# Kernel tuning notes

Measured on AMD Instinct MI355X. Metric: run time of the kernel, lower is better.

The kernel has to match this reference:

```python
import jax, jax.numpy as jnp
import numpy as np

D_MODEL = 2048
N_HEADS = 32
N_KV = 8
D_K = D_MODEL // N_HEADS  # 64
N_REP = N_HEADS // N_KV   # 4


def setup_inputs() -> dict:
    key = jax.random.key(0)
    ks = jax.random.split(key, 5)
    B, T = 2, 2048
    s = 0.02
    return {
        "x": jax.random.normal(ks[0], (B, T, D_MODEL), dtype=jnp.float32),
        "Wq": jax.random.normal(ks[1], (D_MODEL, D_MODEL), dtype=jnp.float32) * s,
        "Wk": jax.random.normal(ks[2], (N_KV * D_K, D_MODEL), dtype=jnp.float32) * s,
        "Wv": jax.random.normal(ks[3], (N_KV * D_K, D_MODEL), dtype=jnp.float32) * s,
        "Wo": jax.random.normal(ks[4], (D_MODEL, D_MODEL), dtype=jnp.float32) * s,
    }


def reference(x, Wq, Wk, Wv, Wo):
    B, T, C = x.shape
    # projections (torch Linear: x @ W.T)
    Q = (x @ Wq.T).reshape(B, T, N_KV, N_REP, D_K)  # group query heads by kv group
    K = (x @ Wk.T).reshape(B, T, N_KV, D_K)
    V = (x @ Wv.T).reshape(B, T, N_KV, D_K)
    scale = 1.0 / jnp.sqrt(jnp.asarray(D_K, dtype=x.dtype))
    # scores: (B, n_kv, n_rep, T, T) == repeated-KV scores without materializing repeats
    scores = jnp.einsum('btgrd,bsgd->bgrts', Q, K) * scale
    causal_mask = jnp.triu(jnp.ones((T, T), dtype=bool), k=1)
    scores = jnp.where(causal_mask, -jnp.inf, scores)
    attn = jax.nn.softmax(scores, axis=-1)
    out = jnp.einsum('bgrts,bsgd->btgrd', attn, V).reshape(B, T, C)
    return out @ Wo.T
```

## Files before the change

kernel.cpp:

```cpp
#include <hip/hip_runtime.h>
#include <hip/hip_bf16.h>

typedef __attribute__((ext_vector_type(8))) short bf16x8;
typedef __attribute__((ext_vector_type(4))) float floatx4;

constexpr int D_MODEL = 2048;
constexpr int N_HEADS = 32;
constexpr int N_KV    = 8;
constexpr int D_K     = 64;
constexpr int B_      = 2;
constexpr int T_      = 2048;
constexpr int BT      = B_ * T_;
constexpr int NQKV    = 3072;

__device__ __forceinline__ unsigned short f2bf(float f) {
    __hip_bfloat16 h = __float2bfloat16(f);
    return *reinterpret_cast<unsigned short*>(&h);
}

__device__ __forceinline__ void gll16(const void* g, void* l) {
    typedef const __attribute__((address_space(1))) unsigned int* gp_t;
    typedef __attribute__((address_space(3))) unsigned int* lp_t;
    __builtin_amdgcn_global_load_lds((gp_t)g, (lp_t)l, 16, 0, 0);
}

__global__ __launch_bounds__(256) void cvt_bf16(
        const float* __restrict__ src, unsigned short* __restrict__ dst, int n4) {
    int i = blockIdx.x * 256 + threadIdx.x;
    if (i < n4) {
        float4 f = reinterpret_cast<const float4*>(src)[i];
        unsigned short u[4] = {f2bf(f.x), f2bf(f.y), f2bf(f.z), f2bf(f.w)};
        reinterpret_cast<uint2*>(dst)[i] = *reinterpret_cast<const uint2*>(u);
    }
}

template<bool B_F32, bool C_F32>
__global__ __launch_bounds__(256) void gemm128(
        const unsigned short* __restrict__ A,
        const void* __restrict__ Bp,
        void* __restrict__ Cp,
        int M, int N, int K) {
    __shared__ unsigned short As[128 * 64];
    __shared__ unsigned short Bs[128 * 64];
    const int t = threadIdx.x;
    const int wave = t >> 6, lane = t & 63;
    const int l16 = lane & 15, quad = lane >> 4;
    const int wm = (wave & 1) * 64, wn = (wave >> 1) * 64;
    const int mtile = blockIdx.y * 128, ntile = blockIdx.x * 128;

    floatx4 acc[4][4] = {};

    for (int k0 = 0; k0 < K; k0 += 64) {
        __syncthreads();
#pragma unroll
        for (int c = 0; c < 4; c++) {
            int s = (c * 4 + wave) * 64 + lane;
            int row = s >> 3, k8 = (s & 7) ^ (row & 7);
            gll16(&A[(size_t)(mtile + row) * K + k0 + k8 * 8], &As[(c * 4 + wave) * 512]);
        }
        if constexpr (!B_F32) {
            const unsigned short* Bb = (const unsigned short*)Bp;
#pragma unroll
            for (int c = 0; c < 4; c++) {
                int s = (c * 4 + wave) * 64 + lane;
                int row = s >> 3, k8 = (s & 7) ^ (row & 7);
                gll16(&Bb[(size_t)(ntile + row) * K + k0 + k8 * 8], &Bs[(c * 4 + wave) * 512]);
            }
        } else {
            const float* Bf = (const float*)Bp;
#pragma unroll
            for (int c = 0; c < 4; c++) {
                int s = c * 256 + t;
                int row = s >> 3, k8 = (s & 7) ^ (row & 7);
                const float* p = &Bf[(size_t)(ntile + row) * K + k0 + k8 * 8];
                float4 f0 = *reinterpret_cast<const float4*>(p);
                float4 f1 = *reinterpret_cast<const float4*>(p + 4);
                unsigned short u[8] = {f2bf(f0.x), f2bf(f0.y), f2bf(f0.z), f2bf(f0.w),
                                       f2bf(f1.x), f2bf(f1.y), f2bf(f1.z), f2bf(f1.w)};
                *reinterpret_cast<uint4*>(&Bs[s * 8]) = *reinterpret_cast<const uint4*>(u);
            }
        }
        __syncthreads();
#pragma unroll
        for (int kc = 0; kc < 2; kc++) {
            bf16x8 af[4], bfr[4];
#pragma unroll
            for (int i = 0; i < 4; i++) {
                int arow = wm + i * 16 + l16;
                af[i] = *reinterpret_cast<const bf16x8*>(
                    &As[(arow * 8 + ((kc * 4 + quad) ^ (arow & 7))) * 8]);
                int brow = wn + i * 16 + l16;
                bfr[i] = *reinterpret_cast<const bf16x8*>(
                    &Bs[(brow * 8 + ((kc * 4 + quad) ^ (brow & 7))) * 8]);
            }
#pragma unroll
            for (int i = 0; i < 4; i++)
#pragma unroll
                for (int jn = 0; jn < 4; jn++)
                    acc[i][jn] = __builtin_amdgcn_mfma_f32_16x16x32_bf16(
                        af[i], bfr[jn], acc[i][jn], 0, 0, 0);
        }
    }
#pragma unroll
    for (int i = 0; i < 4; i++)
#pragma unroll
        for (int jn = 0; jn < 4; jn++)
#pragma unroll
            for (int r = 0; r < 4; r++) {
                int row = mtile + wm + i * 16 + quad * 4 + r;
                int col = ntile + wn + jn * 16 + l16;
                if constexpr (C_F32)
                    ((float*)Cp)[(size_t)row * N + col] = acc[i][jn][r];
                else
                    ((unsigned short*)Cp)[(size_t)row * N + col] = f2bf(acc[i][jn][r]);
            }
}

__global__ __launch_bounds__(256) void vtrans(
        const unsigned short* __restrict__ QKV,
        unsigned short* __restrict__ Vt) {
    __shared__ unsigned short Ts[64][72];
    const int tb = blockIdx.x * 64;
    const int bg = blockIdx.y;
    const int b = bg >> 3, g = bg & 7;
    const int t = threadIdx.x;
#pragma unroll
    for (int it = 0; it < 2; it++) {
        int row = (t >> 3) + it * 32;
        int sl = t & 7;
        *reinterpret_cast<uint4*>(&Ts[row][sl * 8]) =
            *reinterpret_cast<const uint4*>(
                &QKV[(size_t)(b * T_ + tb + row) * NQKV + 2560 + g * 64 + sl * 8]);
    }
    __syncthreads();
#pragma unroll
    for (int it = 0; it < 2; it++) {
        int d = (t >> 3) + it * 32;
        int ks = t & 7;
        unsigned short u[8];
#pragma unroll
        for (int j = 0; j < 8; j++) u[j] = Ts[ks * 8 + j][d];
        *reinterpret_cast<uint4*>(&Vt[((size_t)bg * 64 + d) * T_ + tb + ks * 8]) =
            *reinterpret_cast<const uint4*>(u);
    }
}

__global__ __launch_bounds__(256) void attn2(
        const unsigned short* __restrict__ QKV,
        const unsigned short* __restrict__ Vt,
        unsigned short* __restrict__ O) {
    __shared__ unsigned short Ks[64 * 64];
    __shared__ unsigned short Vs[64 * 64];
    __shared__ unsigned short Ps[4][16 * 72];
    const int j = blockIdx.x;
    const int bh = blockIdx.y;
    const int b = bh >> 5, h = bh & 31;
    const int g = h >> 2;
    const int t = threadIdx.x, wave = t >> 6, lane = t & 63;
    const int l16 = lane & 15, quad = lane >> 4;

    for (int pp = 0; pp < 2; pp++) {
        const int qtl = pp ? (31 - j) : j;
        const int qb0 = qtl * 64;
        const unsigned short* qptr =
            QKV + (size_t)(b * T_ + qb0 + wave * 16 + l16) * NQKV + h * 64;
        bf16x8 qf0 = *reinterpret_cast<const bf16x8*>(qptr + quad * 8);
        bf16x8 qf1 = *reinterpret_cast<const bf16x8*>(qptr + 32 + quad * 8);
        floatx4 o[4] = {};
        float lp[4] = {0.f, 0.f, 0.f, 0.f};
        const int myrow = qb0 + wave * 16 + quad * 4;

        for (int kt = 0; kt <= qtl; kt++) {
            const int kb = kt * 64;
            __syncthreads();
#pragma unroll
            for (int c = 0; c < 2; c++) {
                int s = (c * 4 + wave) * 64 + lane;
                int row = s >> 3, k8 = (s & 7) ^ (row & 7);
                gll16(&QKV[(size_t)(b * T_ + kb + row) * NQKV + 2048 + g * 64 + k8 * 8],
                      &Ks[(c * 4 + wave) * 512]);
                gll16(&Vt[((size_t)(b * 8 + g) * 64 + row) * T_ + kb + k8 * 8],
                      &Vs[(c * 4 + wave) * 512]);
            }
            __syncthreads();

            floatx4 s4[4];
#pragma unroll
            for (int nt = 0; nt < 4; nt++) {
                int krow = nt * 16 + l16;
                bf16x8 b0 = *reinterpret_cast<const bf16x8*>(
                    &Ks[(krow * 8 + (quad ^ (krow & 7))) * 8]);
                bf16x8 b1 = *reinterpret_cast<const bf16x8*>(
                    &Ks[(krow * 8 + ((4 + quad) ^ (krow & 7))) * 8]);
                floatx4 z = {};
                z = __builtin_amdgcn_mfma_f32_16x16x32_bf16(qf0, b0, z, 0, 0, 0);
                s4[nt] = __builtin_amdgcn_mfma_f32_16x16x32_bf16(qf1, b1, z, 0, 0, 0);
            }
            const bool diag = (kt == qtl);
#pragma unroll
            for (int nt = 0; nt < 4; nt++) {
                int key = kb + nt * 16 + l16;
#pragma unroll
                for (int r = 0; r < 4; r++) {
                    float p = __expf(s4[nt][r] * 0.125f);
                    if (diag && key > myrow + r) p = 0.f;
                    lp[r] += p;
                    Ps[wave][(quad * 4 + r) * 72 + nt * 16 + l16] = f2bf(p);
                }
            }
            bf16x8 p0 = *reinterpret_cast<const bf16x8*>(&Ps[wave][l16 * 72 + quad * 8]);
            bf16x8 p1 = *reinterpret_cast<const bf16x8*>(&Ps[wave][l16 * 72 + 32 + quad * 8]);
#pragma unroll
            for (int nt = 0; nt < 4; nt++) {
                int vrow = nt * 16 + l16;
                bf16x8 v0 = *reinterpret_cast<const bf16x8*>(
                    &Vs[(vrow * 8 + (quad ^ (vrow & 7))) * 8]);
                bf16x8 v1 = *reinterpret_cast<const bf16x8*>(
                    &Vs[(vrow * 8 + ((4 + quad) ^ (vrow & 7))) * 8]);
                o[nt] = __builtin_amdgcn_mfma_f32_16x16x32_bf16(p0, v0, o[nt], 0, 0, 0);
                o[nt] = __builtin_amdgcn_mfma_f32_16x16x32_bf16(p1, v1, o[nt], 0, 0, 0);
            }
        }
#pragma unroll
        for (int r = 0; r < 4; r++) {
            float l = lp[r];
#pragma unroll
            for (int off = 8; off >= 1; off >>= 1) l += __shfl_xor(l, off);
            float inv = 1.0f / l;
            int row = b * T_ + qb0 + wave * 16 + quad * 4 + r;
#pragma unroll
            for (int nt = 0; nt < 4; nt++)
                O[(size_t)row * D_MODEL + h * 64 + nt * 16 + l16] = f2bf(o[nt][r] * inv);
        }
    }
}

extern "C" void kernel_launch(void* const* d_in, const int* in_sizes, int n_in,
                              void* d_out, int out_size, void* d_ws, size_t ws_size,
                              hipStream_t stream) {
    const float* x  = (const float*)d_in[0];
    const float* Wq = (const float*)d_in[1];
    const float* Wk = (const float*)d_in[2];
    const float* Wv = (const float*)d_in[3];
    const float* Wo = (const float*)d_in[4];

    unsigned short* xb   = (unsigned short*)d_ws;
    unsigned short* Wqkv = xb + (size_t)BT * D_MODEL;
    unsigned short* QKVo = Wqkv + (size_t)NQKV * D_MODEL;
    unsigned short* Vt   = QKVo + (size_t)BT * NQKV;
    unsigned short* Aw   = xb;

    dim3 blk(256);
    cvt_bf16<<<dim3(BT * D_MODEL / 4 / 256), blk, 0, stream>>>(x, xb, BT * D_MODEL / 4);
    cvt_bf16<<<dim3(D_MODEL * D_MODEL / 4 / 256), blk, 0, stream>>>(
        Wq, Wqkv, D_MODEL * D_MODEL / 4);
    cvt_bf16<<<dim3(512 * D_MODEL / 4 / 256), blk, 0, stream>>>(
        Wk, Wqkv + (size_t)2048 * D_MODEL, 512 * D_MODEL / 4);
    cvt_bf16<<<dim3(512 * D_MODEL / 4 / 256), blk, 0, stream>>>(
        Wv, Wqkv + (size_t)2560 * D_MODEL, 512 * D_MODEL / 4);

    gemm128<false, false><<<dim3(NQKV / 128, BT / 128), blk, 0, stream>>>(
        xb, Wqkv, QKVo, BT, NQKV, D_MODEL);
    vtrans<<<dim3(T_ / 64, B_ * N_KV), blk, 0, stream>>>(QKVo, Vt);
    attn2<<<dim3(16, B_ * N_HEADS), blk, 0, stream>>>(QKVo, Vt, Aw);
    gemm128<true, true><<<dim3(D_MODEL / 128, BT / 128), blk, 0, stream>>>(
        Aw, Wo, d_out, BT, D_MODEL, D_MODEL);
}
```

Before: 302.2 us.

## Share K/V tiles across paired query blocks and pre-convert Wo to bf16

The attention kernel now processes both paired query tiles (j and 31-j) in one pass over the key tiles. Each K/V tile is loaded into LDS once and reused for both query blocks, instead of running two sequential passes that reload the overlapping prefix. S is computed transposed (K as the A operand), so P can be written to LDS with packed stores. The four fp32-to-bf16 conversion kernels are merged into one launch. Wo is converted to bf16 up front so the output GEMM can use direct global-to-LDS loads instead of converting inline. The trade-off is higher register pressure from two sets of accumulators.

```diff
diff --git a/kernel.cpp b/kernel.cpp
--- a/kernel.cpp
+++ b/kernel.cpp
@@ -7,7 +7,6 @@
 constexpr int D_MODEL = 2048;
 constexpr int N_HEADS = 32;
 constexpr int N_KV    = 8;
-constexpr int D_K     = 64;
 constexpr int B_      = 2;
 constexpr int T_      = 2048;
 constexpr int BT      = B_ * T_;
@@ -22,6 +21,22 @@
     typedef const __attribute__((address_space(1))) unsigned int* gp_t;
     typedef __attribute__((address_space(3))) unsigned int* lp_t;
     __builtin_amdgcn_global_load_lds((gp_t)g, (lp_t)l, 16, 0, 0);
+}
+
+__global__ __launch_bounds__(256) void cvt_all(
+        const float* __restrict__ x,  const float* __restrict__ wq,
+        const float* __restrict__ wk, const float* __restrict__ wv,
+        unsigned short* __restrict__ dst) {
+    size_t i4 = (size_t)blockIdx.x * 256 + threadIdx.x;
+    size_t e = i4 * 4;
+    const float* src; size_t off;
+    if (e < 8388608)        { src = x;  off = 0; }
+    else if (e < 12582912)  { src = wq; off = 8388608; }
+    else if (e < 13631488)  { src = wk; off = 12582912; }
+    else                    { src = wv; off = 13631488; }
+    float4 f = *reinterpret_cast<const float4*>(src + (e - off));
+    unsigned short u[4] = {f2bf(f.x), f2bf(f.y), f2bf(f.z), f2bf(f.w)};
+    reinterpret_cast<uint2*>(dst)[i4] = *reinterpret_cast<const uint2*>(u);
 }
 
 __global__ __launch_bounds__(256) void cvt_bf16(
@@ -34,10 +49,10 @@
     }
 }
 
-template<bool B_F32, bool C_F32>
+template<bool C_F32>
 __global__ __launch_bounds__(256) void gemm128(
         const unsigned short* __restrict__ A,
-        const void* __restrict__ Bp,
+        const unsigned short* __restrict__ Bb,
         void* __restrict__ Cp,
         int M, int N, int K) {
     __shared__ unsigned short As[128 * 64];
@@ -57,28 +72,7 @@
             int s = (c * 4 + wave) * 64 + lane;
             int row = s >> 3, k8 = (s & 7) ^ (row & 7);
             gll16(&A[(size_t)(mtile + row) * K + k0 + k8 * 8], &As[(c * 4 + wave) * 512]);
-        }
-        if constexpr (!B_F32) {
-            const unsigned short* Bb = (const unsigned short*)Bp;
-#pragma unroll
-            for (int c = 0; c < 4; c++) {
-                int s = (c * 4 + wave) * 64 + lane;
-                int row = s >> 3, k8 = (s & 7) ^ (row & 7);
-                gll16(&Bb[(size_t)(ntile + row) * K + k0 + k8 * 8], &Bs[(c * 4 + wave) * 512]);
-            }
-        } else {
-            const float* Bf = (const float*)Bp;
-#pragma unroll
-            for (int c = 0; c < 4; c++) {
-                int s = c * 256 + t;
-                int row = s >> 3, k8 = (s & 7) ^ (row & 7);
-                const float* p = &Bf[(size_t)(ntile + row) * K + k0 + k8 * 8];
-                float4 f0 = *reinterpret_cast<const float4*>(p);
-                float4 f1 = *reinterpret_cast<const float4*>(p + 4);
-                unsigned short u[8] = {f2bf(f0.x), f2bf(f0.y), f2bf(f0.z), f2bf(f0.w),
-                                       f2bf(f1.x), f2bf(f1.y), f2bf(f1.z), f2bf(f1.w)};
-                *reinterpret_cast<uint4*>(&Bs[s * 8]) = *reinterpret_cast<const uint4*>(u);
-            }
+            gll16(&Bb[(size_t)(ntile + row) * K + k0 + k8 * 8], &Bs[(c * 4 + wave) * 512]);
         }
         __syncthreads();
 #pragma unroll
@@ -145,92 +139,136 @@
     }
 }
 
-__global__ __launch_bounds__(256) void attn2(
+__global__ __launch_bounds__(256) void attn3(
         const unsigned short* __restrict__ QKV,
         const unsigned short* __restrict__ Vt,
         unsigned short* __restrict__ O) {
     __shared__ unsigned short Ks[64 * 64];
     __shared__ unsigned short Vs[64 * 64];
     __shared__ unsigned short Ps[4][16 * 72];
-    const int j = blockIdx.x;
+    const int j  = blockIdx.x;
     const int bh = blockIdx.y;
     const int b = bh >> 5, h = bh & 31;
     const int g = h >> 2;
     const int t = threadIdx.x, wave = t >> 6, lane = t & 63;
     const int l16 = lane & 15, quad = lane >> 4;
 
-    for (int pp = 0; pp < 2; pp++) {
-        const int qtl = pp ? (31 - j) : j;
-        const int qb0 = qtl * 64;
-        const unsigned short* qptr =
-            QKV + (size_t)(b * T_ + qb0 + wave * 16 + l16) * NQKV + h * 64;
-        bf16x8 qf0 = *reinterpret_cast<const bf16x8*>(qptr + quad * 8);
-        bf16x8 qf1 = *reinterpret_cast<const bf16x8*>(qptr + 32 + quad * 8);
-        floatx4 o[4] = {};
-        float lp[4] = {0.f, 0.f, 0.f, 0.f};
-        const int myrow = qb0 + wave * 16 + quad * 4;
-
-        for (int kt = 0; kt <= qtl; kt++) {
-            const int kb = kt * 64;
-            __syncthreads();
-#pragma unroll
-            for (int c = 0; c < 2; c++) {
-                int s = (c * 4 + wave) * 64 + lane;
-                int row = s >> 3, k8 = (s & 7) ^ (row & 7);
-                gll16(&QKV[(size_t)(b * T_ + kb + row) * NQKV + 2048 + g * 64 + k8 * 8],
-                      &Ks[(c * 4 + wave) * 512]);
-                gll16(&Vt[((size_t)(b * 8 + g) * 64 + row) * T_ + kb + k8 * 8],
-                      &Vs[(c * 4 + wave) * 512]);
-            }
-            __syncthreads();
-
-            floatx4 s4[4];
-#pragma unroll
-            for (int nt = 0; nt < 4; nt++) {
-                int krow = nt * 16 + l16;
-                bf16x8 b0 = *reinterpret_cast<const bf16x8*>(
-                    &Ks[(krow * 8 + (quad ^ (krow & 7))) * 8]);
-                bf16x8 b1 = *reinterpret_cast<const bf16x8*>(
-                    &Ks[(krow * 8 + ((4 + quad) ^ (krow & 7))) * 8]);
-                floatx4 z = {};
-                z = __builtin_amdgcn_mfma_f32_16x16x32_bf16(qf0, b0, z, 0, 0, 0);
-                s4[nt] = __builtin_amdgcn_mfma_f32_16x16x32_bf16(qf1, b1, z, 0, 0, 0);
-            }
-            const bool diag = (kt == qtl);
-#pragma unroll
-            for (int nt = 0; nt < 4; nt++) {
-                int key = kb + nt * 16 + l16;
-#pragma unroll
-                for (int r = 0; r < 4; r++) {
-                    float p = __expf(s4[nt][r] * 0.125f);
-                    if (diag && key > myrow + r) p = 0.f;
-                    lp[r] += p;
-                    Ps[wave][(quad * 4 + r) * 72 + nt * 16 + l16] = f2bf(p);
-                }
-            }
+    const int qtlA = j, qtlB = 31 - j;
+    const int qA = qtlA * 64 + wave * 16 + l16;
+    const int qB = qtlB * 64 + wave * 16 + l16;
+
+    const unsigned short* qpA = QKV + (size_t)(b * T_ + qA) * NQKV + h * 64;
+    const unsigned short* qpB = QKV + (size_t)(b * T_ + qB) * NQKV + h * 64;
+    bf16x8 qA0 = *reinterpret_cast<const bf16x8*>(qpA + quad * 8);
+    bf16x8 qA1 = *reinterpret_cast<const bf16x8*>(qpA + 32 + quad * 8);
+    bf16x8 qB0 = *reinterpret_cast<const bf16x8*>(qpB + quad * 8);
+    bf16x8 qB1 = *reinterpret_cast<const bf16x8*>(qpB + 32 + quad * 8);
+
+    floatx4 oA[4] = {}, oB[4] = {};
+    float lpA = 0.f, lpB = 0.f;
+
+    for (int kt = 0; kt <= qtlB; kt++) {
+        const int kb = kt * 64;
+        const bool doA = (kt <= qtlA);
+        __syncthreads();
+#pragma unroll
+        for (int c = 0; c < 2; c++) {
+            int s = (c * 4 + wave) * 64 + lane;
+            int row = s >> 3, k8 = (s & 7) ^ (row & 7);
+            gll16(&QKV[(size_t)(b * T_ + kb + row) * NQKV + 2048 + g * 64 + k8 * 8],
+                  &Ks[(c * 4 + wave) * 512]);
+            gll16(&Vt[((size_t)(b * 8 + g) * 64 + row) * T_ + kb + k8 * 8],
+                  &Vs[(c * 4 + wave) * 512]);
+        }
+        __syncthreads();
+
+        floatx4 sA[4], sB[4];
+#pragma unroll
+        for (int nt = 0; nt < 4; nt++) {
+            int krow = nt * 16 + l16;
+            bf16x8 k0 = *reinterpret_cast<const bf16x8*>(
+                &Ks[(krow * 8 + (quad ^ (krow & 7))) * 8]);
+            bf16x8 k1 = *reinterpret_cast<const bf16x8*>(
+                &Ks[(krow * 8 + ((4 + quad) ^ (krow & 7))) * 8]);
+            floatx4 z = {};
+            z = __builtin_amdgcn_mfma_f32_16x16x32_bf16(k0, qB0, z, 0, 0, 0);
+            sB[nt] = __builtin_amdgcn_mfma_f32_16x16x32_bf16(k1, qB1, z, 0, 0, 0);
+            if (doA) {
+                floatx4 za = {};
+                za = __builtin_amdgcn_mfma_f32_16x16x32_bf16(k0, qA0, za, 0, 0, 0);
+                sA[nt] = __builtin_amdgcn_mfma_f32_16x16x32_bf16(k1, qA1, za, 0, 0, 0);
+            }
+        }
+
+        const bool diagB = (kt == qtlB), diagA = (kt == qtlA);
+#pragma unroll
+        for (int nt = 0; nt < 4; nt++) {
+            unsigned short u[4];
+#pragma unroll
+            for (int r = 0; r < 4; r++) {
+                float p = __expf(sB[nt][r] * 0.125f);
+                if (diagB && (kb + nt * 16 + quad * 4 + r) > qB) p = 0.f;
+                lpB += p;
+                u[r] = f2bf(p);
+            }
+            *reinterpret_cast<uint2*>(&Ps[wave][l16 * 72 + nt * 16 + quad * 4]) =
+                *reinterpret_cast<const uint2*>(u);
+        }
+        {
             bf16x8 p0 = *reinterpret_cast<const bf16x8*>(&Ps[wave][l16 * 72 + quad * 8]);
             bf16x8 p1 = *reinterpret_cast<const bf16x8*>(&Ps[wave][l16 * 72 + 32 + quad * 8]);
 #pragma unroll
-            for (int nt = 0; nt < 4; nt++) {
-                int vrow = nt * 16 + l16;
+            for (int dt = 0; dt < 4; dt++) {
+                int vrow = dt * 16 + l16;
                 bf16x8 v0 = *reinterpret_cast<const bf16x8*>(
                     &Vs[(vrow * 8 + (quad ^ (vrow & 7))) * 8]);
                 bf16x8 v1 = *reinterpret_cast<const bf16x8*>(
                     &Vs[(vrow * 8 + ((4 + quad) ^ (vrow & 7))) * 8]);
-                o[nt] = __builtin_amdgcn_mfma_f32_16x16x32_bf16(p0, v0, o[nt], 0, 0, 0);
-                o[nt] = __builtin_amdgcn_mfma_f32_16x16x32_bf16(p1, v1, o[nt], 0, 0, 0);
-            }
-        }
-#pragma unroll
-        for (int r = 0; r < 4; r++) {
-            float l = lp[r];
-#pragma unroll
-            for (int off = 8; off >= 1; off >>= 1) l += __shfl_xor(l, off);
-            float inv = 1.0f / l;
-            int row = b * T_ + qb0 + wave * 16 + quad * 4 + r;
-#pragma unroll
-            for (int nt = 0; nt < 4; nt++)
-                O[(size_t)row * D_MODEL + h * 64 + nt * 16 + l16] = f2bf(o[nt][r] * inv);
+                oB[dt] = __builtin_amdgcn_mfma_f32_16x16x32_bf16(p0, v0, oB[dt], 0, 0, 0);
+                oB[dt] = __builtin_amdgcn_mfma_f32_16x16x32_bf16(p1, v1, oB[dt], 0, 0, 0);
+            }
+        }
+        if (doA) {
+#pragma unroll
+            for (int nt = 0; nt < 4; nt++) {
+                unsigned short u[4];
+#pragma unroll
+                for (int r = 0; r < 4; r++) {
+                    float p = __expf(sA[nt][r] * 0.125f);
+                    if (diagA && (kb + nt * 16 + quad * 4 + r) > qA) p = 0.f;
+                    lpA += p;
+                    u[r] = f2bf(p);
+                }
+                *reinterpret_cast<uint2*>(&Ps[wave][l16 * 72 + nt * 16 + quad * 4]) =
+                    *reinterpret_cast<const uint2*>(u);
+            }
+            bf16x8 p0 = *reinterpret_cast<const bf16x8*>(&Ps[wave][l16 * 72 + quad * 8]);
+            bf16x8 p1 = *reinterpret_cast<const bf16x8*>(&Ps[wave][l16 * 72 + 32 + quad * 8]);
+#pragma unroll
+            for (int dt = 0; dt < 4; dt++) {
+                int vrow = dt * 16 + l16;
+                bf16x8 v0 = *reinterpret_cast<const bf16x8*>(
+                    &Vs[(vrow * 8 + (quad ^ (vrow & 7))) * 8]);
+                bf16x8 v1 = *reinterpret_cast<const bf16x8*>(
+                    &Vs[(vrow * 8 + ((4 + quad) ^ (vrow & 7))) * 8]);
+                oA[dt] = __builtin_amdgcn_mfma_f32_16x16x32_bf16(p0, v0, oA[dt], 0, 0, 0);
+                oA[dt] = __builtin_amdgcn_mfma_f32_16x16x32_bf16(p1, v1, oA[dt], 0, 0, 0);
+            }
+        }
+    }
+
+    lpA += __shfl_xor(lpA, 16); lpA += __shfl_xor(lpA, 32);
+    lpB += __shfl_xor(lpB, 16); lpB += __shfl_xor(lpB, 32);
+#pragma unroll
+    for (int r = 0; r < 4; r++) {
+        float invA = 1.0f / __shfl(lpA, quad * 4 + r);
+        float invB = 1.0f / __shfl(lpB, quad * 4 + r);
+        int rowA = b * T_ + qtlA * 64 + wave * 16 + quad * 4 + r;
+        int rowB = b * T_ + qtlB * 64 + wave * 16 + quad * 4 + r;
+#pragma unroll
+        for (int dt = 0; dt < 4; dt++) {
+            O[(size_t)rowA * D_MODEL + h * 64 + dt * 16 + l16] = f2bf(oA[dt][r] * invA);
+            O[(size_t)rowB * D_MODEL + h * 64 + dt * 16 + l16] = f2bf(oB[dt][r] * invB);
         }
     }
 }
@@ -249,20 +287,16 @@
     unsigned short* QKVo = Wqkv + (size_t)NQKV * D_MODEL;
     unsigned short* Vt   = QKVo + (size_t)BT * NQKV;
     unsigned short* Aw   = xb;
+    unsigned short* Wob  = Wqkv;
 
     dim3 blk(256);
-    cvt_bf16<<<dim3(BT * D_MODEL / 4 / 256), blk, 0, stream>>>(x, xb, BT * D_MODEL / 4);
+    cvt_all<<<dim3(14336), blk, 0, stream>>>(x, Wq, Wk, Wv, xb);
+    gemm128<false><<<dim3(NQKV / 128, BT / 128), blk, 0, stream>>>(
+        xb, Wqkv, QKVo, BT, NQKV, D_MODEL);
     cvt_bf16<<<dim3(D_MODEL * D_MODEL / 4 / 256), blk, 0, stream>>>(
-        Wq, Wqkv, D_MODEL * D_MODEL / 4);
-    cvt_bf16<<<dim3(512 * D_MODEL / 4 / 256), blk, 0, stream>>>(
-        Wk, Wqkv + (size_t)2048 * D_MODEL, 512 * D_MODEL / 4);
-    cvt_bf16<<<dim3(512 * D_MODEL / 4 / 256), blk, 0, stream>>>(
-        Wv, Wqkv + (size_t)2560 * D_MODEL, 512 * D_MODEL / 4);
-
-    gemm128<false, false><<<dim3(NQKV / 128, BT / 128), blk, 0, stream>>>(
-        xb, Wqkv, QKVo, BT, NQKV, D_MODEL);
+        Wo, Wob, D_MODEL * D_MODEL / 4);
     vtrans<<<dim3(T_ / 64, B_ * N_KV), blk, 0, stream>>>(QKVo, Vt);
-    attn2<<<dim3(16, B_ * N_HEADS), blk, 0, stream>>>(QKVo, Vt, Aw);
-    gemm128<true, true><<<dim3(D_MODEL / 128, BT / 128), blk, 0, stream>>>(
-        Aw, Wo, d_out, BT, D_MODEL, D_MODEL);
-}
+    attn3<<<dim3(16, B_ * N_HEADS), blk, 0, stream>>>(QKVo, Vt, Aw);
+    gemm128<true><<<dim3(D_MODEL / 128, BT / 128), blk, 0, stream>>>(
+        Aw, Wob, d_out, BT, D_MODEL, D_MODEL);
+}
```

Result: slower. 314.9 us (+4.2%).
